# Performance work log

Hardware: AMD Instinct MI355X
Metric: run time of the kernel (lower is better)

## Reference

```python
import jax, jax.numpy as jnp
import numpy as np

V = 6890          # SMPL vertex count
RAYS, POINTS = 256, 64
LATENT_DIM = 16
RES_HI, RES_LO = 10, 4


def posenc(x, res):
    # NeRF-style encoding: [x, sin(2^k x), cos(2^k x)] for k in 0..res-1 -> D*(1+2*res)
    freqs = 2.0 ** jnp.arange(res, dtype=x.dtype)            # [res]
    xf = x[..., None, :] * freqs[:, None]                    # [..., res, D]
    n = x.shape[:-1]
    s = jnp.sin(xf).reshape(*n, -1)
    c = jnp.cos(xf).reshape(*n, -1)
    return jnp.concatenate([x, s, c], axis=-1)


def setup_inputs() -> dict:
    key = jax.random.key(0)
    ks = jax.random.split(key, 12)
    inp = {}
    inp['pts'] = jax.random.normal(ks[0], (RAYS, POINTS, 6), jnp.float32)
    inp['keypoints'] = jax.random.normal(ks[1], (V, 3), jnp.float32)
    # invertible per-vertex 4x4 transforms: identity + small noise, stored [4,4,V]
    noise = 0.1 * jax.random.normal(ks[2], (4, 4, V), jnp.float32)
    inp['trans_kp'] = jnp.eye(4, dtype=jnp.float32)[:, :, None] + noise
    inp['neighbors'] = jax.random.randint(ks[3], (V, 7), 0, V, jnp.int32)
    inp['rest_pose'] = jax.random.normal(ks[4], (V, 3), jnp.float32)
    inp['latent'] = jax.random.normal(ks[5], (V, LATENT_DIM), jnp.float32)
    d_in = 7 * ((2 * RES_HI + 1) * 4 + LATENT_DIM)  # 700
    inp['W1'] = 0.05 * jax.random.normal(ks[6], (d_in, 256), jnp.float32)
    inp['b1'] = jnp.zeros((256,), jnp.float32)
    inp['W2'] = 0.05 * jax.random.normal(ks[7], (256, 256), jnp.float32)
    inp['b2'] = jnp.zeros((256,), jnp.float32)
    inp['W3'] = 0.05 * jax.random.normal(ks[8], (256, 256), jnp.float32)
    inp['b3'] = jnp.zeros((256,), jnp.float32)
    return inp


def reference(pts, keypoints, trans_kp, neighbors, rest_pose, latent,
              W1, b1, W2, b2, W3, b3):
    rays, points, _ = pts.shape
    p, view_dir = jnp.split(pts, 2, axis=-1)
    p = p.reshape(rays * points, 3)                          # [N,3]

    # brute-force 1-NN of p into keypoints
    d2 = ((p * p).sum(-1, keepdims=True)
          - 2.0 * p @ keypoints.T
          + (keypoints * keypoints).sum(-1))                 # [N,V]
    knn_index = jnp.argmin(d2, axis=1)                       # [N]

    # inverse transforms, keep rotation part: [3,3,V]
    T = jnp.linalg.inv(jnp.transpose(trans_kp, (2, 0, 1)))   # [V,4,4]
    R = jnp.transpose(T, (1, 2, 0))[:3, :3]                  # [3,3,V]

    vidx = neighbors[knn_index]                              # [N,7]
    vdist = p[:, None, :] - keypoints[vidx]                  # [N,7,3]

    diff = p - keypoints[knn_index]                          # [N,3]
    Rg = R[:, :, knn_index]                                  # [3,3,N]
    direction = jnp.einsum('ijn,nj->ni', Rg, diff)           # [N,3]
    nrm = jnp.linalg.norm(direction, axis=-1, keepdims=True)
    direction = direction / jnp.maximum(nrm, 1e-12)

    vfeat = jnp.concatenate(
        [rest_pose[vidx].reshape(-1, 21),
         jnp.linalg.norm(vdist, axis=-1)], axis=-1)          # [N,28]
    lfeat = latent[vidx].reshape(-1, 7 * latent.shape[1])    # [N,112]

    h = jnp.concatenate([posenc(vfeat, RES_HI), lfeat], -1)  # [N,700]
    h = jax.nn.relu(h @ W1 + b1)
    h = jax.nn.relu(h @ W2 + b2)
    h = h @ W3 + b3                                          # [N,256]

    out = jnp.concatenate([h, posenc(direction, RES_LO)], -1)  # [N,283]
    return out.reshape(rays, points, -1)
```

## Files before the change

kernel.cpp:

```cpp
#include <hip/hip_runtime.h>
#include <hip/hip_bf16.h>
#include <math.h>

#define V_N   6890
#define N_PTS 16384
#define D_IN  700
#define D_INP 704
#define D_HID 256
#define D_OUT 283
#define GAP_EPS 1e-4f

#define RINV4_OFF 0
#define KP4_OFF   82688
#define RP4_OFF   110272
#define WT1_OFF   2267792
#define WT2_OFF   2357904
#define WT3_OFF   2390672
#define X_OFF     2423440

typedef __attribute__((ext_vector_type(8))) short short8;
typedef __attribute__((ext_vector_type(4))) float f32x4;

__device__ __forceinline__ unsigned short f2bf(float f) {
    unsigned int u = __builtin_bit_cast(unsigned int, f);
    u += 0x7fffu + ((u >> 16) & 1u);
    return (unsigned short)(u >> 16);
}

__device__ __forceinline__ float fsin(float x) {
    return __builtin_amdgcn_sinf(__builtin_amdgcn_fractf(x * 0.15915494309189535f));
}
__device__ __forceinline__ float fcos(float x) {
    return __builtin_amdgcn_cosf(__builtin_amdgcn_fractf(x * 0.15915494309189535f));
}

__device__ __forceinline__ void glds16(const void* g, void* l) {
    __builtin_amdgcn_global_load_lds(
        (const __attribute__((address_space(1))) void*)g,
        (__attribute__((address_space(3))) void*)l, 16, 0, 0);
}

__device__ __forceinline__ int swzoff(int r, int sub) {
    return ((r << 2) | (sub ^ ((r >> 1) & 3))) << 4;
}

__device__ __forceinline__ int rescan64(const float* __restrict__ pts,
                                        const float4* __restrict__ kp4,
                                        int nn, int lane) {
    double pxd = (double)pts[nn*6+0], pyd = (double)pts[nn*6+1], pzd = (double)pts[nn*6+2];
    double ppd = pxd*pxd + pyd*pyd + pzd*pzd;
    double best = 1e300; int bbi = 0x7fffffff;
    for (int jj = lane; jj < V_N; jj += 64) {
        float4 k = kp4[jj];
        double kx = (double)k.x, ky = (double)k.y, kz = (double)k.z;
        double d = ppd - 2.0*(pxd*kx + pyd*ky + pzd*kz) + (kx*kx + ky*ky + kz*kz);
        if (d < best || (d == best && jj < bbi)) { best = d; bbi = jj; }
    }
#pragma unroll
    for (int off = 32; off >= 1; off >>= 1) {
        double od = __shfl_xor(best, off);
        int    oi = __shfl_xor(bbi, off);
        if (od < best || (od == best && oi < bbi)) { best = od; bbi = oi; }
    }
    return bbi;
}

#define PREP_BLOCKS 27
__global__ __launch_bounds__(256) void prep_wconv_kernel(
    const float* __restrict__ trans, const float* __restrict__ keyp,
    const float* __restrict__ restp,
    float4* __restrict__ rinv4, float4* __restrict__ kp4, float4* __restrict__ rp4,
    const float* __restrict__ W1, const float* __restrict__ W2,
    const float* __restrict__ W3, unsigned short* __restrict__ wt1,
    unsigned short* __restrict__ wt2, unsigned short* __restrict__ wt3)
{
    if (blockIdx.x < PREP_BLOCKS) {
        int v = blockIdx.x * 256 + threadIdx.x;
        if (v >= V_N) return;
        float m[16];
#pragma unroll
        for (int i = 0; i < 16; ++i) m[i] = trans[i * V_N + v];

        float i0  =  m[5]*m[10]*m[15] - m[5]*m[11]*m[14] - m[9]*m[6]*m[15] + m[9]*m[7]*m[14] + m[13]*m[6]*m[11] - m[13]*m[7]*m[10];
        float i4  = -m[4]*m[10]*m[15] + m[4]*m[11]*m[14] + m[8]*m[6]*m[15] - m[8]*m[7]*m[14] - m[12]*m[6]*m[11] + m[12]*m[7]*m[10];
        float i8  =  m[4]*m[9]*m[15]  - m[4]*m[11]*m[13] - m[8]*m[5]*m[15] + m[8]*m[7]*m[13] + m[12]*m[5]*m[11] - m[12]*m[7]*m[9];
        float i12 = -m[4]*m[9]*m[14]  + m[4]*m[10]*m[13] + m[8]*m[5]*m[14] - m[8]*m[6]*m[13] - m[12]*m[5]*m[10] + m[12]*m[6]*m[9];
        float i1  = -m[1]*m[10]*m[15] + m[1]*m[11]*m[14] + m[9]*m[2]*m[15] - m[9]*m[3]*m[14] - m[13]*m[2]*m[11] + m[13]*m[3]*m[10];
        float i5  =  m[0]*m[10]*m[15] - m[0]*m[11]*m[14] - m[8]*m[2]*m[15] + m[8]*m[3]*m[14] + m[12]*m[2]*m[11] - m[12]*m[3]*m[10];
        float i9  = -m[0]*m[9]*m[15]  + m[0]*m[11]*m[13] + m[8]*m[1]*m[15] - m[8]*m[3]*m[13] - m[12]*m[1]*m[11] + m[12]*m[3]*m[9];
        float i2  =  m[1]*m[6]*m[15]  - m[1]*m[7]*m[14]  - m[5]*m[2]*m[15] + m[5]*m[3]*m[14] + m[13]*m[2]*m[7]  - m[13]*m[3]*m[6];
        float i6  = -m[0]*m[6]*m[15]  + m[0]*m[7]*m[14]  + m[4]*m[2]*m[15] - m[4]*m[3]*m[14] - m[12]*m[2]*m[7]  + m[12]*m[3]*m[6];
        float i10 =  m[0]*m[5]*m[15]  - m[0]*m[7]*m[13]  - m[4]*m[1]*m[15] + m[4]*m[3]*m[13] + m[12]*m[1]*m[7]  - m[12]*m[3]*m[5];

        float det = m[0]*i0 + m[1]*i4 + m[2]*i8 + m[3]*i12;
        float id = 1.0f / det;
        rinv4[v*3+0] = make_float4(i0*id, i1*id, i2*id, i4*id);
        rinv4[v*3+1] = make_float4(i5*id, i6*id, i8*id, i9*id);
        rinv4[v*3+2] = make_float4(i10*id, 0.0f, 0.0f, 0.0f);

        float kx = keyp[v*3], ky = keyp[v*3+1], kz = keyp[v*3+2];
        kp4[v] = make_float4(kx, ky, kz, kx*kx + ky*ky + kz*kz);
        rp4[v] = make_float4(restp[v*3], restp[v*3+1], restp[v*3+2], 0.0f);
    } else {
        int idx = (blockIdx.x - PREP_BLOCKS) * 256 + threadIdx.x;
        const int N1 = 256 * D_INP;
        const int N2 = 256 * 256;
        if (idx < N1) {
            int n = idx / D_INP, k = idx - n * D_INP;
            float v = (k < D_IN) ? W1[k * 256 + n] : 0.0f;
            wt1[n * D_INP + k] = f2bf(v);
        } else if (idx < N1 + N2) {
            int t = idx - N1;
            int n = t >> 8, k = t & 255;
            wt2[n * 256 + k] = f2bf(W2[k * 256 + n]);
        } else if (idx < N1 + 2 * N2) {
            int t = idx - N1 - N2;
            int n = t >> 8, k = t & 255;
            wt3[n * 256 + k] = f2bf(W3[k * 256 + n]);
        }
    }
}

__global__ __launch_bounds__(256) void feat_kernel(
    const float* __restrict__ pts, const int* __restrict__ neigh,
    const float* __restrict__ latent, const float4* __restrict__ rinv4,
    const float4* __restrict__ kp4, const float4* __restrict__ rp4,
    unsigned short* __restrict__ X, float* __restrict__ out)
{
    __shared__ float s_vf[4][2][29];
    __shared__ float s_dir[4][2][4];

    int t = threadIdx.x;
    int w = t >> 6, lane = t & 63;
    int n0 = blockIdx.x * 8 + w * 2;

    float pxA2 = 2.0f*pts[n0*6+0],     pyA2 = 2.0f*pts[n0*6+1],     pzA2 = 2.0f*pts[n0*6+2];
    float pxB2 = 2.0f*pts[(n0+1)*6+0], pyB2 = 2.0f*pts[(n0+1)*6+1], pzB2 = 2.0f*pts[(n0+1)*6+2];

    float m1A = 1e30f, m2A = 1e30f; int biA = 0x7fffffff;
    float m1B = 1e30f, m2B = 1e30f; int biB = 0x7fffffff;

    for (int j = lane; j < 6912; j += 64) {
        int jc = min(j, V_N - 1);
        float4 kk = kp4[jc];
        float dA = kk.w - (pxA2*kk.x + pyA2*kk.y + pzA2*kk.z);
        float dB = kk.w - (pxB2*kk.x + pyB2*kk.y + pzB2*kk.z);
        if (j >= V_N) { dA = 1e30f; dB = 1e30f; }
        bool ltA = dA < m1A;
        m2A = ltA ? m1A : fminf(m2A, dA);
        biA = ltA ? j : biA;
        m1A = fminf(m1A, dA);
        bool ltB = dB < m1B;
        m2B = ltB ? m1B : fminf(m2B, dB);
        biB = ltB ? j : biB;
        m1B = fminf(m1B, dB);
    }
#pragma unroll
    for (int off = 1; off <= 32; off <<= 1) {
        float o1 = __shfl_xor(m1A, off), o2 = __shfl_xor(m2A, off);
        int   ob = __shfl_xor(biA, off);
        float nm2 = fminf(fminf(m2A, o2), fmaxf(m1A, o1));
        bool take = (o1 < m1A) || (o1 == m1A && ob < biA);
        biA = take ? ob : biA;  m1A = fminf(m1A, o1);  m2A = nm2;

        o1 = __shfl_xor(m1B, off);  o2 = __shfl_xor(m2B, off);
        ob = __shfl_xor(biB, off);
        nm2 = fminf(fminf(m2B, o2), fmaxf(m1B, o1));
        take = (o1 < m1B) || (o1 == m1B && ob < biB);
        biB = take ? ob : biB;  m1B = fminf(m1B, o1);  m2B = nm2;
    }
    if (m2A - m1A < GAP_EPS) biA = rescan64(pts, kp4, n0,     lane);
    if (m2B - m1B < GAP_EPS) biB = rescan64(pts, kp4, n0 + 1, lane);

    int p = lane >> 5, j = lane & 31;
    int np = n0 + p;
    int k8 = p ? biB : biA;
    float px = pts[np*6+0], py = pts[np*6+1], pz = pts[np*6+2];

    int v7 = 0;
    if (j < 7) {
        v7 = neigh[k8*7 + j];
        float4 kq = kp4[v7];
        float4 rq = rp4[v7];
        float dx = px - kq.x, dy = py - kq.y, dz = pz - kq.z;
        s_vf[w][p][j*3+0] = rq.x;
        s_vf[w][p][j*3+1] = rq.y;
        s_vf[w][p][j*3+2] = rq.z;
        s_vf[w][p][21+j]  = sqrtf(dx*dx + dy*dy + dz*dz);
    } else if (j == 7) {
        float4 kq = kp4[k8];
        float ddx = px - kq.x, ddy = py - kq.y, ddz = pz - kq.z;
        float4 R0 = rinv4[k8*3+0];
        float4 R1 = rinv4[k8*3+1];
        float4 R2 = rinv4[k8*3+2];
        float d0 = R0.x*ddx + R0.y*ddy + R0.z*ddz;
        float d1 = R0.w*ddx + R1.x*ddy + R1.y*ddz;
        float d2 = R1.z*ddx + R1.w*ddy + R2.x*ddz;
        float nrm = fmaxf(sqrtf(d0*d0 + d1*d1 + d2*d2), 1e-12f);
        s_dir[w][p][0] = d0/nrm; s_dir[w][p][1] = d1/nrm; s_dir[w][p][2] = d2/nrm;
    }

#pragma unroll
    for (int pp = 0; pp < 2; ++pp) {
        int n = n0 + pp;
        float dir0 = s_dir[w][pp][0];
        float dir1 = s_dir[w][pp][1];
        float dir2 = s_dir[w][pp][2];

        if (lane < 27) {
            float val;
            if (lane < 3) {
                val = (lane == 0) ? dir0 : (lane == 1) ? dir1 : dir2;
            } else {
                int tt = (lane < 15) ? lane - 3 : lane - 15;
                int m = tt % 3;
                float db = (m == 0) ? dir0 : (m == 1) ? dir1 : dir2;
                float a = db * (float)(1 << (tt/3));
                val = (lane < 15) ? fsin(a) : fcos(a);
            }
            out[(size_t)n*D_OUT + 256 + lane] = val;
        }

#pragma unroll
        for (int it = 0; it < 3; ++it) {
            int base = it * 256 + (lane << 2);
            bool in_range = base < D_INP;
            int region = (base < 28) ? 0 : (base < 308) ? 1 : (base < 588) ? 2
                       : (base < 700) ? 3 : 4;

            int t0 = (region == 1) ? base - 28 : (region == 2) ? base - 308 : 0;
            int q = t0 / 28;
            int r = t0 - q * 28;
            float f0 = (float)(1 << q);
            float a[4];
#pragma unroll
            for (int jj = 0; jj < 4; ++jj) {
                int rj; float fj;
                if (region == 0) { rj = base + jj; fj = 1.0f; }
                else if (region <= 2) {
                    rj = r + jj; fj = f0;
                    if (rj >= 28) { rj -= 28; fj = f0 * 2.0f; }
                } else { rj = 0; fj = 0.0f; }
                a[jj] = s_vf[w][pp][rj] * fj;
            }
            int idxc = (region == 3) ? (base - 588) >> 4 : 0;
            int vL = __shfl(v7, pp*32 + idxc);

            unsigned short r0, r1, r2, r3;
            if (region == 0) {
                r0 = f2bf(a[0]); r1 = f2bf(a[1]); r2 = f2bf(a[2]); r3 = f2bf(a[3]);
            } else if (region == 1) {
                r0 = f2bf(fsin(a[0])); r1 = f2bf(fsin(a[1]));
                r2 = f2bf(fsin(a[2])); r3 = f2bf(fsin(a[3]));
            } else if (region == 2) {
                r0 = f2bf(fcos(a[0])); r1 = f2bf(fcos(a[1]));
                r2 = f2bf(fcos(a[2])); r3 = f2bf(fcos(a[3]));
            } else if (region == 3) {
                int t3 = base - 588;
                float4 lv = *(const float4*)&latent[vL * 16 + (t3 & 15)];
                r0 = f2bf(lv.x); r1 = f2bf(lv.y); r2 = f2bf(lv.z); r3 = f2bf(lv.w);
            } else {
                r0 = r1 = r2 = r3 = 0;
            }
            if (in_range)
                *(ushort4*)&X[(size_t)n * D_INP + base] = make_ushort4(r0, r1, r2, r3);
        }
    }
}

#define HLD 264
__global__ __launch_bounds__(512) void mlp_kernel(
    const unsigned short* __restrict__ X,
    const unsigned short* __restrict__ wt1,
    const unsigned short* __restrict__ wt2,
    const unsigned short* __restrict__ wt3,
    const float* __restrict__ b1, const float* __restrict__ b2,
    const float* __restrict__ b3, float* __restrict__ out)
{
    __shared__ unsigned short As[64 * 32];
    __shared__ unsigned short Ws[256 * 32];
    __shared__ unsigned short H1[64 * HLD];
    __shared__ unsigned short H2[64 * HLD];

    int t = threadIdx.x, l = t & 63, w = t >> 6;
    int bm = blockIdx.x * 64;
    int mbase = (w >> 2) * 32, nbase = (w & 3) * 64;
    int lrow = l & 15, lk = (l >> 4) * 8, sub = l >> 4;
    int col0 = l & 15, rquad = (l >> 4) * 4;

    f32x4 acc[2][4];
    short8 af[2], bf[4];

#pragma unroll
    for (int mi = 0; mi < 2; ++mi)
#pragma unroll
        for (int ni = 0; ni < 4; ++ni) acc[mi][ni] = {0.f, 0.f, 0.f, 0.f};

    for (int k0 = 0; k0 < D_INP; k0 += 32) {
        if (t < 256) {
            int r = t >> 2;
            int sg = (t & 3) ^ ((r >> 1) & 3);
            glds16(X + (size_t)(bm + r) * D_INP + k0 + sg * 8, (char*)As + t * 16);
        }
#pragma unroll
        for (int i = 0; i < 2; ++i) {
            int c = i * 512 + t;
            int r = c >> 2;
            int sg = (c & 3) ^ ((r >> 1) & 3);
            glds16(wt1 + (size_t)r * D_INP + k0 + sg * 8, (char*)Ws + (size_t)c * 16);
        }
        __syncthreads();
#pragma unroll
        for (int mi = 0; mi < 2; ++mi)
            af[mi] = *(const short8*)((const char*)As + swzoff(mbase + mi*16 + lrow, sub));
#pragma unroll
        for (int ni = 0; ni < 4; ++ni)
            bf[ni] = *(const short8*)((const char*)Ws + swzoff(nbase + ni*16 + lrow, sub));
#pragma unroll
        for (int mi = 0; mi < 2; ++mi)
#pragma unroll
            for (int ni = 0; ni < 4; ++ni)
                acc[mi][ni] = __builtin_amdgcn_mfma_f32_16x16x32_bf16(
                    af[mi], bf[ni], acc[mi][ni], 0, 0, 0);
        __syncthreads();
    }
#pragma unroll
    for (int mi = 0; mi < 2; ++mi)
#pragma unroll
        for (int ni = 0; ni < 4; ++ni) {
            int col = nbase + ni * 16 + col0;
            float bv = b1[col];
#pragma unroll
            for (int r = 0; r < 4; ++r) {
                int row = mbase + mi * 16 + rquad + r;
                H1[row * HLD + col] = f2bf(fmaxf(acc[mi][ni][r] + bv, 0.0f));
            }
        }
    __syncthreads();

#pragma unroll
    for (int mi = 0; mi < 2; ++mi)
#pragma unroll
        for (int ni = 0; ni < 4; ++ni) acc[mi][ni] = {0.f, 0.f, 0.f, 0.f};

    for (int k0 = 0; k0 < D_HID; k0 += 32) {
#pragma unroll
        for (int i = 0; i < 2; ++i) {
            int c = i * 512 + t;
            int r = c >> 2;
            int sg = (c & 3) ^ ((r >> 1) & 3);
            glds16(wt2 + (size_t)r * D_HID + k0 + sg * 8, (char*)Ws + (size_t)c * 16);
        }
        __syncthreads();
#pragma unroll
        for (int mi = 0; mi < 2; ++mi)
            af[mi] = *(const short8*)&H1[(mbase + mi * 16 + lrow) * HLD + k0 + lk];
#pragma unroll
        for (int ni = 0; ni < 4; ++ni)
            bf[ni] = *(const short8*)((const char*)Ws + swzoff(nbase + ni*16 + lrow, sub));
#pragma unroll
        for (int mi = 0; mi < 2; ++mi)
#pragma unroll
            for (int ni = 0; ni < 4; ++ni)
                acc[mi][ni] = __builtin_amdgcn_mfma_f32_16x16x32_bf16(
                    af[mi], bf[ni], acc[mi][ni], 0, 0, 0);
        __syncthreads();
    }
#pragma unroll
    for (int mi = 0; mi < 2; ++mi)
#pragma unroll
        for (int ni = 0; ni < 4; ++ni) {
            int col = nbase + ni * 16 + col0;
            float bv = b2[col];
#pragma unroll
            for (int r = 0; r < 4; ++r) {
                int row = mbase + mi * 16 + rquad + r;
                H2[row * HLD + col] = f2bf(fmaxf(acc[mi][ni][r] + bv, 0.0f));
            }
        }
    __syncthreads();

#pragma unroll
    for (int mi = 0; mi < 2; ++mi)
#pragma unroll
        for (int ni = 0; ni < 4; ++ni) acc[mi][ni] = {0.f, 0.f, 0.f, 0.f};

    for (int k0 = 0; k0 < D_HID; k0 += 32) {
#pragma unroll
        for (int i = 0; i < 2; ++i) {
            int c = i * 512 + t;
            int r = c >> 2;
            int sg = (c & 3) ^ ((r >> 1) & 3);
            glds16(wt3 + (size_t)r * D_HID + k0 + sg * 8, (char*)Ws + (size_t)c * 16);
        }
        __syncthreads();
#pragma unroll
        for (int mi = 0; mi < 2; ++mi)
            af[mi] = *(const short8*)&H2[(mbase + mi * 16 + lrow) * HLD + k0 + lk];
#pragma unroll
        for (int ni = 0; ni < 4; ++ni)
            bf[ni] = *(const short8*)((const char*)Ws + swzoff(nbase + ni*16 + lrow, sub));
#pragma unroll
        for (int mi = 0; mi < 2; ++mi)
#pragma unroll
            for (int ni = 0; ni < 4; ++ni)
                acc[mi][ni] = __builtin_amdgcn_mfma_f32_16x16x32_bf16(
                    af[mi], bf[ni], acc[mi][ni], 0, 0, 0);
        __syncthreads();
    }
#pragma unroll
    for (int mi = 0; mi < 2; ++mi)
#pragma unroll
        for (int ni = 0; ni < 4; ++ni) {
            int col = nbase + ni * 16 + col0;
            float bv = b3[col];
#pragma unroll
            for (int r = 0; r < 4; ++r) {
                int row = bm + mbase + mi * 16 + rquad + r;
                out[(size_t)row * D_OUT + col] = acc[mi][ni][r] + bv;
            }
        }
}

extern "C" void kernel_launch(void* const* d_in, const int* in_sizes, int n_in,
                              void* d_out, int out_size, void* d_ws, size_t ws_size,
                              hipStream_t stream) {
    const float* pts    = (const float*)d_in[0];
    const float* keyp   = (const float*)d_in[1];
    const float* trans  = (const float*)d_in[2];
    const int*   neigh  = (const int*)d_in[3];
    const float* restp  = (const float*)d_in[4];
    const float* latent = (const float*)d_in[5];
    const float* W1     = (const float*)d_in[6];
    const float* b1     = (const float*)d_in[7];
    const float* W2     = (const float*)d_in[8];
    const float* b2     = (const float*)d_in[9];
    const float* W3     = (const float*)d_in[10];
    const float* b3     = (const float*)d_in[11];
    float* out = (float*)d_out;

    float* wsf = (float*)d_ws;
    float4*         rinv4 = (float4*)(wsf + RINV4_OFF);
    float4*         kp4   = (float4*)(wsf + KP4_OFF);
    float4*         rp4   = (float4*)(wsf + RP4_OFF);
    unsigned short* wt1   = (unsigned short*)(wsf + WT1_OFF);
    unsigned short* wt2   = (unsigned short*)(wsf + WT2_OFF);
    unsigned short* wt3   = (unsigned short*)(wsf + WT3_OFF);
    unsigned short* X     = (unsigned short*)(wsf + X_OFF);

    int wconv_blocks = (256*D_INP + 2*256*256 + 255) / 256;
    prep_wconv_kernel<<<PREP_BLOCKS + wconv_blocks, 256, 0, stream>>>(
        trans, keyp, restp, rinv4, kp4, rp4, W1, W2, W3, wt1, wt2, wt3);
    feat_kernel<<<N_PTS/8, 256, 0, stream>>>(pts, neigh, latent, rinv4,
                                             kp4, rp4, X, out);
    mlp_kernel<<<N_PTS/64, 512, 0, stream>>>(X, wt1, wt2, wt3, b1, b2, b3, out);
}
```

Measured before the change: 197.9 us.

## Stage keypoints in LDS for NN search and double-buffer MLP tile loads

The nearest-neighbor scan now loads keypoint chunks into shared memory with async global-to-LDS copies, shared by all four waves of a block. Its inner loop uses fused multiply-adds and fmed3 to track the top two distances. The three MLP GEMM loops switch to double-buffered LDS tiles, so the next K-slice loads while MFMAs run on the current one. The next layer's first weight tile is also prefetched during the epilogue. This cuts redundant global keypoint reads and hides load latency, at the cost of more LDS use and block-wide syncs in the feature kernel.

```diff
diff --git a/kernel.cpp b/kernel.cpp
--- a/kernel.cpp
+++ b/kernel.cpp
@@ -121,12 +121,15 @@
     }
 }
 
+#define FCHUNK 864
+#define NFCH   8
 __global__ __launch_bounds__(256) void feat_kernel(
     const float* __restrict__ pts, const int* __restrict__ neigh,
     const float* __restrict__ latent, const float4* __restrict__ rinv4,
     const float4* __restrict__ kp4, const float4* __restrict__ rp4,
     unsigned short* __restrict__ X, float* __restrict__ out)
 {
+    __shared__ float4 s_kp[FCHUNK];
     __shared__ float s_vf[4][2][29];
     __shared__ float s_dir[4][2][4];
 
@@ -134,27 +137,46 @@
     int w = t >> 6, lane = t & 63;
     int n0 = blockIdx.x * 8 + w * 2;
 
-    float pxA2 = 2.0f*pts[n0*6+0],     pyA2 = 2.0f*pts[n0*6+1],     pzA2 = 2.0f*pts[n0*6+2];
-    float pxB2 = 2.0f*pts[(n0+1)*6+0], pyB2 = 2.0f*pts[(n0+1)*6+1], pzB2 = 2.0f*pts[(n0+1)*6+2];
+    float pxA = pts[n0*6+0],     pyA = pts[n0*6+1],     pzA = pts[n0*6+2];
+    float pxB = pts[(n0+1)*6+0], pyB = pts[(n0+1)*6+1], pzB = pts[(n0+1)*6+2];
+    float pxA2n = -2.0f*pxA, pyA2n = -2.0f*pyA, pzA2n = -2.0f*pzA;
+    float pxB2n = -2.0f*pxB, pyB2n = -2.0f*pyB, pzB2n = -2.0f*pzB;
 
     float m1A = 1e30f, m2A = 1e30f; int biA = 0x7fffffff;
     float m1B = 1e30f, m2B = 1e30f; int biB = 0x7fffffff;
 
-    for (int j = lane; j < 6912; j += 64) {
-        int jc = min(j, V_N - 1);
-        float4 kk = kp4[jc];
-        float dA = kk.w - (pxA2*kk.x + pyA2*kk.y + pzA2*kk.z);
-        float dB = kk.w - (pxB2*kk.x + pyB2*kk.y + pzB2*kk.z);
-        if (j >= V_N) { dA = 1e30f; dB = 1e30f; }
-        bool ltA = dA < m1A;
-        m2A = ltA ? m1A : fminf(m2A, dA);
-        biA = ltA ? j : biA;
-        m1A = fminf(m1A, dA);
-        bool ltB = dB < m1B;
-        m2B = ltB ? m1B : fminf(m2B, dB);
-        biB = ltB ? j : biB;
-        m1B = fminf(m1B, dB);
-    }
+    for (int c = 0; c < NFCH; ++c) {
+        int vbase = c * FCHUNK;
+#pragma unroll
+        for (int k = 0; k < 3; ++k)
+            glds16(kp4 + vbase + t + k*256, (char*)s_kp + (size_t)(t + k*256)*16);
+        if (t < FCHUNK - 768)
+            glds16(kp4 + vbase + t + 768, (char*)s_kp + (size_t)(t + 768)*16);
+        __syncthreads();
+
+        int nv = min(V_N - vbase, FCHUNK);
+#pragma unroll 4
+        for (int i = lane; i < nv; i += 64) {
+            float4 kk = s_kp[i];
+            int j = vbase + i;
+            float dA = __builtin_fmaf(pxA2n, kk.x,
+                       __builtin_fmaf(pyA2n, kk.y,
+                       __builtin_fmaf(pzA2n, kk.z, kk.w)));
+            float dB = __builtin_fmaf(pxB2n, kk.x,
+                       __builtin_fmaf(pyB2n, kk.y,
+                       __builtin_fmaf(pzB2n, kk.z, kk.w)));
+            bool ltA = dA < m1A;
+            biA = ltA ? j : biA;
+            m2A = __builtin_amdgcn_fmed3f(m1A, m2A, dA);
+            m1A = fminf(m1A, dA);
+            bool ltB = dB < m1B;
+            biB = ltB ? j : biB;
+            m2B = __builtin_amdgcn_fmed3f(m1B, m2B, dB);
+            m1B = fminf(m1B, dB);
+        }
+        __syncthreads();
+    }
+
 #pragma unroll
     for (int off = 1; off <= 32; off <<= 1) {
         float o1 = __shfl_xor(m1A, off), o2 = __shfl_xor(m2A, off);
@@ -173,9 +195,8 @@
     if (m2B - m1B < GAP_EPS) biB = rescan64(pts, kp4, n0 + 1, lane);
 
     int p = lane >> 5, j = lane & 31;
-    int np = n0 + p;
     int k8 = p ? biB : biA;
-    float px = pts[np*6+0], py = pts[np*6+1], pz = pts[np*6+2];
+    float px = p ? pxB : pxA, py = p ? pyB : pyA, pz = p ? pzB : pzA;
 
     int v7 = 0;
     if (j < 7) {
@@ -277,8 +298,8 @@
     const float* __restrict__ b1, const float* __restrict__ b2,
     const float* __restrict__ b3, float* __restrict__ out)
 {
-    __shared__ unsigned short As[64 * 32];
-    __shared__ unsigned short Ws[256 * 32];
+    __shared__ unsigned short As[2][64 * 32];
+    __shared__ unsigned short Ws[2][256 * 32];
     __shared__ unsigned short H1[64 * HLD];
     __shared__ unsigned short H2[64 * HLD];
 
@@ -291,31 +312,44 @@
     f32x4 acc[2][4];
     short8 af[2], bf[4];
 
-#pragma unroll
-    for (int mi = 0; mi < 2; ++mi)
-#pragma unroll
-        for (int ni = 0; ni < 4; ++ni) acc[mi][ni] = {0.f, 0.f, 0.f, 0.f};
-
-    for (int k0 = 0; k0 < D_INP; k0 += 32) {
+    auto stageA = [&](int buf, int k0) {
         if (t < 256) {
-            int r = t >> 2;
-            int sg = (t & 3) ^ ((r >> 1) & 3);
-            glds16(X + (size_t)(bm + r) * D_INP + k0 + sg * 8, (char*)As + t * 16);
-        }
+            int r = t >> 2, sg = (t & 3) ^ ((r >> 1) & 3);
+            glds16(X + (size_t)(bm + r) * D_INP + k0 + sg * 8,
+                   (char*)As[buf] + t * 16);
+        }
+    };
+    auto stageW = [&](int buf, const unsigned short* wsrc, int ld, int k0) {
 #pragma unroll
         for (int i = 0; i < 2; ++i) {
             int c = i * 512 + t;
-            int r = c >> 2;
-            int sg = (c & 3) ^ ((r >> 1) & 3);
-            glds16(wt1 + (size_t)r * D_INP + k0 + sg * 8, (char*)Ws + (size_t)c * 16);
-        }
-        __syncthreads();
-#pragma unroll
-        for (int mi = 0; mi < 2; ++mi)
-            af[mi] = *(const short8*)((const char*)As + swzoff(mbase + mi*16 + lrow, sub));
+            int r = c >> 2, sg = (c & 3) ^ ((r >> 1) & 3);
+            glds16(wsrc + (size_t)r * ld + k0 + sg * 8,
+                   (char*)Ws[buf] + (size_t)c * 16);
+        }
+    };
+
+#pragma unroll
+    for (int mi = 0; mi < 2; ++mi)
+#pragma unroll
+        for (int ni = 0; ni < 4; ++ni) acc[mi][ni] = {0.f, 0.f, 0.f, 0.f};
+
+    stageA(0, 0);
+    stageW(0, wt1, D_INP, 0);
+    __syncthreads();
+    const int NK1 = D_INP / 32;
+    for (int ks = 0; ks < NK1; ++ks) {
+        int cur = ks & 1;
+        if (ks + 1 < NK1) {
+            stageA(cur ^ 1, (ks + 1) * 32);
+            stageW(cur ^ 1, wt1, D_INP, (ks + 1) * 32);
+        }
+#pragma unroll
+        for (int mi = 0; mi < 2; ++mi)
+            af[mi] = *(const short8*)((const char*)As[cur] + swzoff(mbase + mi*16 + lrow, sub));
 #pragma unroll
         for (int ni = 0; ni < 4; ++ni)
-            bf[ni] = *(const short8*)((const char*)Ws + swzoff(nbase + ni*16 + lrow, sub));
+            bf[ni] = *(const short8*)((const char*)Ws[cur] + swzoff(nbase + ni*16 + lrow, sub));
 #pragma unroll
         for (int mi = 0; mi < 2; ++mi)
 #pragma unroll
@@ -324,6 +358,7 @@
                     af[mi], bf[ni], acc[mi][ni], 0, 0, 0);
         __syncthreads();
     }
+    stageW(0, wt2, D_HID, 0);
 #pragma unroll
     for (int mi = 0; mi < 2; ++mi)
 #pragma unroll
@@ -343,21 +378,16 @@
 #pragma unroll
         for (int ni = 0; ni < 4; ++ni) acc[mi][ni] = {0.f, 0.f, 0.f, 0.f};
 
-    for (int k0 = 0; k0 < D_HID; k0 += 32) {
-#pragma unroll
-        for (int i = 0; i < 2; ++i) {
-            int c = i * 512 + t;
-            int r = c >> 2;
-            int sg = (c & 3) ^ ((r >> 1) & 3);
-            glds16(wt2 + (size_t)r * D_HID + k0 + sg * 8, (char*)Ws + (size_t)c * 16);
-        }
-        __syncthreads();
-#pragma unroll
-        for (int mi = 0; mi < 2; ++mi)
-            af[mi] = *(const short8*)&H1[(mbase + mi * 16 + lrow) * HLD + k0 + lk];
+    const int NK2 = D_HID / 32;
+    for (int ks = 0; ks < NK2; ++ks) {
+        int cur = ks & 1;
+        if (ks + 1 < NK2) stageW(cur ^ 1, wt2, D_HID, (ks + 1) * 32);
+#pragma unroll
+        for (int mi = 0; mi < 2; ++mi)
+            af[mi] = *(const short8*)&H1[(mbase + mi * 16 + lrow) * HLD + ks * 32 + lk];
 #pragma unroll
         for (int ni = 0; ni < 4; ++ni)
-            bf[ni] = *(const short8*)((const char*)Ws + swzoff(nbase + ni*16 + lrow, sub));
+            bf[ni] = *(const short8*)((const char*)Ws[cur] + swzoff(nbase + ni*16 + lrow, sub));
 #pragma unroll
         for (int mi = 0; mi < 2; ++mi)
 #pragma unroll
@@ -366,6 +396,7 @@
                     af[mi], bf[ni], acc[mi][ni], 0, 0, 0);
         __syncthreads();
     }
+    stageW(0, wt3, D_HID, 0);
 #pragma unroll
     for (int mi = 0; mi < 2; ++mi)
 #pragma unroll
@@ -385,21 +416,15 @@
 #pragma unroll
         for (int ni = 0; ni < 4; ++ni) acc[mi][ni] = {0.f, 0.f, 0.f, 0.f};
 
-    for (int k0 = 0; k0 < D_HID; k0 += 32) {
-#pragma unroll
-        for (int i = 0; i < 2; ++i) {
-            int c = i * 512 + t;
-            int r = c >> 2;
-            int sg = (c & 3) ^ ((r >> 1) & 3);
-            glds16(wt3 + (size_t)r * D_HID + k0 + sg * 8, (char*)Ws + (size_t)c * 16);
-        }
-        __syncthreads();
-#pragma unroll
-        for (int mi = 0; mi < 2; ++mi)
-            af[mi] = *(const short8*)&H2[(mbase + mi * 16 + lrow) * HLD + k0 + lk];
+    for (int ks = 0; ks < NK2; ++ks) {
+        int cur = ks & 1;
+        if (ks + 1 < NK2) stageW(cur ^ 1, wt3, D_HID, (ks + 1) * 32);
+#pragma unroll
+        for (int mi = 0; mi < 2; ++mi)
+            af[mi] = *(const short8*)&H2[(mbase + mi * 16 + lrow) * HLD + ks * 32 + lk];
 #pragma unroll
         for (int ni = 0; ni < 4; ++ni)
-            bf[ni] = *(const short8*)((const char*)Ws + swzoff(nbase + ni*16 + lrow, sub));
+            bf[ni] = *(const short8*)((const char*)Ws[cur] + swzoff(nbase + ni*16 + lrow, sub));
 #pragma unroll
         for (int mi = 0; mi < 2; ++mi)
 #pragma unroll
```

Measured after the change: 182.4 us. 7.8% less time.
